# Kernel tuning notes

Hardware: AMD Instinct MI355X
Metric: run time of the kernel (lower is better)

The kernel has to match this reference:

```python
import jax, jax.numpy as jnp
import numpy as np

INPUT_SZ = 16
HPF = 32  # hidden_per_feat_sz
INTERACTIONS = [(0, 1), (2, 3), (4, 5), (6, 7)]
N_INT = len(INTERACTIONS)
INPUT_SIZE = INPUT_SZ + 2 * N_INT          # 24
HIDDEN = (INPUT_SZ + N_INT) * HPF          # 640
BATCH, SEQ = 128, 512

# static masks, faithful to the torch code (note: only even-indexed interactions
# get U_mask rows, exactly as the original loop `range(0, len(interactions), 2)`)
_Um = np.zeros((INPUT_SIZE, HIDDEN), np.float32)
for i in range(INPUT_SZ):
    _Um[i, i * HPF:(i + 1) * HPF] = 1
for i in range(0, N_INT, 2):
    _Um[i + INPUT_SZ, i * HPF:(i + 1) * HPF] = 1
    _Um[i + INPUT_SZ + 1, i * HPF:(i + 1) * HPF] = 1
U_MASK = jnp.asarray(_Um)
V_MASK = jnp.asarray(np.kron(np.eye(INPUT_SZ + N_INT, dtype=np.float32),
                             np.ones((HPF, HPF), np.float32)))
FEAT_SEQ = np.array(list(range(INPUT_SZ)) + [f for p in INTERACTIONS for f in p])


def setup_inputs() -> dict:
    key = jax.random.key(0)
    ks = jax.random.split(key, 13)
    stdv = 1.0 / np.sqrt(HIDDEN)
    u = lambda k, s: jax.random.uniform(k, s, jnp.float32, -stdv, stdv)
    inp = {"x": jax.random.normal(ks[0], (BATCH, SEQ, INPUT_SZ), jnp.float32)}
    names = ["i", "f", "c", "o"]
    for j, n in enumerate(names):
        inp[f"U_{n}"] = u(ks[1 + 3 * j], (INPUT_SIZE, HIDDEN))
        inp[f"V_{n}"] = u(ks[2 + 3 * j], (HIDDEN, HIDDEN))
        inp[f"b_{n}"] = u(ks[3 + 3 * j], (HIDDEN,))
    return inp


def reference(x, U_i, V_i, b_i, U_f, V_f, b_f, U_c, V_c, b_c, U_o, V_o, b_o):
    # gather masked-feature view of inputs once: [B, T, INPUT_SIZE]
    xg = x[:, :, FEAT_SEQ]
    # precompute masked, gate-concatenated weights (i|f|c|o)
    Ucat = jnp.concatenate([U_i * U_MASK, U_f * U_MASK,
                            U_c * U_MASK, U_o * U_MASK], axis=1)   # [in, 4H]
    Vcat = jnp.concatenate([V_i * V_MASK, V_f * V_MASK,
                            V_c * V_MASK, V_o * V_MASK], axis=1)   # [H, 4H]
    bcat = jnp.concatenate([b_i, b_f, b_c, b_o])                   # [4H]
    # input contribution for all timesteps in one GEMM: [B, T, 4H]
    xU = jnp.einsum('bti,ig->btg', xg, Ucat) + bcat

    h0 = jnp.zeros((x.shape[0], HIDDEN), x.dtype)
    c0 = jnp.zeros_like(h0)

    def step(carry, xu_t):
        h, c = carry
        gates = xu_t + h @ Vcat
        i_t, f_t, g_t, o_t = jnp.split(gates, 4, axis=-1)
        c = jax.nn.sigmoid(f_t) * c + jax.nn.sigmoid(i_t) * jnp.tanh(g_t)
        h = jax.nn.sigmoid(o_t) * jnp.tanh(c)
        return (h, c), h

    (h_t, c_t), hs = jax.lax.scan(step, (h0, c0), jnp.swapaxes(xU, 0, 1))
    hidden_seq = jnp.swapaxes(hs, 0, 1)  # [B, T, H]
    return hidden_seq, (h_t, c_t)
```

## Files before the change

kernel.cpp:

```cpp
#include <hip/hip_runtime.h>


#define TT 512
#define HN 640
#define BN 128

typedef float f2 __attribute__((ext_vector_type(2)));

__device__ __forceinline__ float rl(float v, int s) {
  return __int_as_float(__builtin_amdgcn_readlane(__float_as_int(v), s));
}

__global__ __attribute__((amdgpu_flat_work_group_size(64, 64),
                          amdgpu_waves_per_eu(2, 4)))
void lstm_kernel(
    const float* __restrict__ x,
    const float* __restrict__ Ui, const float* __restrict__ Vi, const float* __restrict__ bi,
    const float* __restrict__ Uf, const float* __restrict__ Vf, const float* __restrict__ bf,
    const float* __restrict__ Uc, const float* __restrict__ Vc, const float* __restrict__ bc,
    const float* __restrict__ Uo, const float* __restrict__ Vo, const float* __restrict__ bo,
    float* __restrict__ out) {
  __shared__ __align__(16) float hsh[64];

  const int unit = blockIdx.x;
  const int lane = threadIdx.x;
  const int j = unit >> 7;
  const int b = unit & 127;
  const int gp = lane >> 5;
  const int n = lane & 31;
  const int col = j * 32 + n;

  const float* UG1 = gp ? Uc : Ui;
  const float* UG2 = gp ? Uo : Uf;
  const float* VG1 = gp ? Vc : Vi;
  const float* VG2 = gp ? Vo : Vf;
  const float* bG1 = gp ? bc : bi;
  const float* bG2 = gp ? bo : bf;

  const float LOG2E = 1.44269504088896340736f;
  const float B1 = gp ? (-2.f * LOG2E) : -LOG2E;
  const float B2 = -LOG2E;
  const float Ac1 = gp ? 2.f : 1.f;
  const float Cc1 = gp ? -1.f : 0.f;

  float w11 = 0.f, w21 = 0.f, w12 = 0.f, w22 = 0.f;
  int f1 = 0, f2i = 0;
  if (j < 16) {
    f1 = f2i = j;
    w11 = UG1[j * HN + col];
    w12 = UG2[j * HN + col];
    if (j == 0) {
      w11 += UG1[16 * HN + col]; w12 += UG2[16 * HN + col];
      w21  = UG1[17 * HN + col]; w22  = UG2[17 * HN + col];
      f2i = 1;
    } else if (j == 2) {
      w11 += UG1[18 * HN + col]; w12 += UG2[18 * HN + col];
      w21  = UG1[19 * HN + col]; w22  = UG2[19 * HN + col];
      f2i = 3;
    }
  }
  const float ws11 = B1 * w11, ws21 = B1 * w21, bs1 = B1 * bG1[col];
  const float ws12 = B2 * w12, ws22 = B2 * w22, bs2 = B2 * bG2[col];

  f2 wA[16], wB[16];
#pragma unroll
  for (int kp = 0; kp < 16; ++kp) {
    wA[kp].x = B1 * VG1[(j * 32 + 2 * kp) * HN + col];
    wA[kp].y = B1 * VG1[(j * 32 + 2 * kp + 1) * HN + col];
    wB[kp].x = B2 * VG2[(j * 32 + 2 * kp) * HN + col];
    wB[kp].y = B2 * VG2[(j * 32 + 2 * kp + 1) * HN + col];
  }
#pragma unroll
  for (int kp = 0; kp < 16; ++kp) {
    asm volatile("" : "+v"(wA[kp]), "+v"(wB[kp]));
  }

  float h = 0.f, c = 0.f;
  int ob = b * TT * HN + col;
#pragma unroll 1
  for (int i = 0; i < 8; ++i) {
    const int t = i * 64 + lane;
    float xc1 = x[(b * TT + t) * 16 + f1];
    float xc2 = x[(b * TT + t) * 16 + f2i];
    asm volatile("" : "+v"(xc1), "+v"(xc2));
    for (int s = 0; s < 64; ++s) {
      const float x1 = rl(xc1, s);
      const float x2 = rl(xc2, s);
      const float sx1 = fmaf(x2, ws21, fmaf(x1, ws11, bs1));
      const float sx2 = fmaf(x2, ws22, fmaf(x1, ws12, bs2));
      hsh[lane] = h;
      __builtin_amdgcn_wave_barrier();
      f2 hp[16];
      __builtin_memcpy(hp, hsh, 128);
      __builtin_amdgcn_wave_barrier();
      f2 aA = {sx1, 0.f}, aB = {sx2, 0.f};
#pragma unroll
      for (int kp = 0; kp < 16; ++kp) {
        aA = __builtin_elementwise_fma(wA[kp], hp[kp], aA);
        aB = __builtin_elementwise_fma(wB[kp], hp[kp], aB);
      }
      const float a1 = aA.x + aA.y;
      const float a2 = aB.x + aB.y;
      const float e1 = __builtin_amdgcn_exp2f(a1);
      const float e2 = __builtin_amdgcn_exp2f(a2);
      const float g1 = fmaf(Ac1, __builtin_amdgcn_rcpf(1.f + e1), Cc1);
      const float g2 = __builtin_amdgcn_rcpf(1.f + e2);
      const float p1 = __shfl_xor(g1, 32);
      const float p2 = __shfl_xor(g2, 32);
      c = fmaf(g2, c, g1 * p1);
      const float tc = fmaf(
          2.f,
          __builtin_amdgcn_rcpf(1.f + __builtin_amdgcn_exp2f(-2.f * LOG2E * c)),
          -1.f);
      h = p2 * tc;
      if (lane < 32) out[ob] = h;
      ob += HN;
    }
  }
  if (lane < 32) {
    out[BN * TT * HN + b * HN + col] = h;
    out[BN * TT * HN + BN * HN + b * HN + col] = c;
  }
}

extern "C" void kernel_launch(void* const* d_in, const int* in_sizes, int n_in,
                              void* d_out, int out_size, void* d_ws, size_t ws_size,
                              hipStream_t stream) {
  (void)in_sizes; (void)n_in; (void)d_ws; (void)ws_size; (void)out_size;
  const float* x  = (const float*)d_in[0];
  const float* Ui = (const float*)d_in[1];
  const float* Vi = (const float*)d_in[2];
  const float* bi = (const float*)d_in[3];
  const float* Uf = (const float*)d_in[4];
  const float* Vf = (const float*)d_in[5];
  const float* bf = (const float*)d_in[6];
  const float* Uc = (const float*)d_in[7];
  const float* Vc = (const float*)d_in[8];
  const float* bc = (const float*)d_in[9];
  const float* Uo = (const float*)d_in[10];
  const float* Vo = (const float*)d_in[11];
  const float* bo = (const float*)d_in[12];
  float* out = (float*)d_out;

  dim3 grid(2560);
  dim3 block(64);
  hipLaunchKernelGGL(lstm_kernel, grid, block, 0, stream,
                     x, Ui, Vi, bi, Uf, Vf, bf, Uc, Vc, bc, Uo, Vo, bo, out);
}
```

Measured before the change: 385.0 us.

## Hand-write LSTM timestep loop in inline assembly with LDS-staged inputs

The per-timestep recurrence is replaced by a hand-scheduled inline-asm loop. Inputs are staged in LDS and fetched with ds_read2, replacing readlane. The next 64-step x chunk is prefetched into registers, and the half-wave exchange uses ds_bpermute. Outputs go through buffer_store with an out-of-range offset that masks the upper half-wave, removing the branch. The intent is to shorten the serial per-step latency chain, at the cost of fragile hardcoded registers, s_nop hazard handling and dropping the waves_per_eu hint.

```diff
diff --git a/kernel.cpp b/kernel.cpp
--- a/kernel.cpp
+++ b/kernel.cpp
@@ -6,13 +6,9 @@
 #define BN 128
 
 typedef float f2 __attribute__((ext_vector_type(2)));
-
-__device__ __forceinline__ float rl(float v, int s) {
-  return __int_as_float(__builtin_amdgcn_readlane(__float_as_int(v), s));
-}
-
-__global__ __attribute__((amdgpu_flat_work_group_size(64, 64),
-                          amdgpu_waves_per_eu(2, 4)))
+typedef unsigned int u32x4 __attribute__((ext_vector_type(4)));
+
+__global__ __attribute__((amdgpu_flat_work_group_size(64, 64)))
 void lstm_kernel(
     const float* __restrict__ x,
     const float* __restrict__ Ui, const float* __restrict__ Vi, const float* __restrict__ bi,
@@ -20,7 +16,7 @@
     const float* __restrict__ Uc, const float* __restrict__ Vc, const float* __restrict__ bc,
     const float* __restrict__ Uo, const float* __restrict__ Vo, const float* __restrict__ bo,
     float* __restrict__ out) {
-  __shared__ __align__(16) float hsh[64];
+  __shared__ __align__(16) float hsh[192];
 
   const int unit = blockIdx.x;
   const int lane = threadIdx.x;
@@ -70,53 +66,151 @@
     wB[kp].x = B2 * VG2[(j * 32 + 2 * kp) * HN + col];
     wB[kp].y = B2 * VG2[(j * 32 + 2 * kp + 1) * HN + col];
   }
-#pragma unroll
-  for (int kp = 0; kp < 16; ++kp) {
-    asm volatile("" : "+v"(wA[kp]), "+v"(wB[kp]));
-  }
+
+  const unsigned zb    = (unsigned)(unsigned long long)&hsh[0];
+  const unsigned laddr = zb + (unsigned)lane * 4u;
+  const unsigned xbase = zb + 256u;
+  const unsigned swz   = (unsigned)((lane ^ 32) & 63) * 4u;
+
+  const unsigned out_bytes = (unsigned)((BN * TT * HN + 2 * BN * HN) * 4);
+  const unsigned long long outa = (unsigned long long)out;
+  u32x4 srd;
+  srd.x = (unsigned)outa;
+  srd.y = (unsigned)(outa >> 32);
+  srd.z = out_bytes;
+  srd.w = 0x00020000u;
+  unsigned voff = (lane < 32) ? (unsigned)((b * TT * HN + col) * 4)
+                              : 0x60000000u;
 
   float h = 0.f, c = 0.f;
-  int ob = b * TT * HN + col;
+
+  float nx1 = x[(b * TT + lane) * 16 + f1];
+  float nx2 = x[(b * TT + lane) * 16 + f2i];
+
 #pragma unroll 1
   for (int i = 0; i < 8; ++i) {
-    const int t = i * 64 + lane;
-    float xc1 = x[(b * TT + t) * 16 + f1];
-    float xc2 = x[(b * TT + t) * 16 + f2i];
-    asm volatile("" : "+v"(xc1), "+v"(xc2));
-    for (int s = 0; s < 64; ++s) {
-      const float x1 = rl(xc1, s);
-      const float x2 = rl(xc2, s);
-      const float sx1 = fmaf(x2, ws21, fmaf(x1, ws11, bs1));
-      const float sx2 = fmaf(x2, ws22, fmaf(x1, ws12, bs2));
-      hsh[lane] = h;
-      __builtin_amdgcn_wave_barrier();
-      f2 hp[16];
-      __builtin_memcpy(hp, hsh, 128);
-      __builtin_amdgcn_wave_barrier();
-      f2 aA = {sx1, 0.f}, aB = {sx2, 0.f};
-#pragma unroll
-      for (int kp = 0; kp < 16; ++kp) {
-        aA = __builtin_elementwise_fma(wA[kp], hp[kp], aA);
-        aB = __builtin_elementwise_fma(wB[kp], hp[kp], aB);
-      }
-      const float a1 = aA.x + aA.y;
-      const float a2 = aB.x + aB.y;
-      const float e1 = __builtin_amdgcn_exp2f(a1);
-      const float e2 = __builtin_amdgcn_exp2f(a2);
-      const float g1 = fmaf(Ac1, __builtin_amdgcn_rcpf(1.f + e1), Cc1);
-      const float g2 = __builtin_amdgcn_rcpf(1.f + e2);
-      const float p1 = __shfl_xor(g1, 32);
-      const float p2 = __shfl_xor(g2, 32);
-      c = fmaf(g2, c, g1 * p1);
-      const float tc = fmaf(
-          2.f,
-          __builtin_amdgcn_rcpf(1.f + __builtin_amdgcn_exp2f(-2.f * LOG2E * c)),
-          -1.f);
-      h = p2 * tc;
-      if (lane < 32) out[ob] = h;
-      ob += HN;
+    hsh[64 + lane]  = nx1;
+    hsh[128 + lane] = nx2;
+    if (i < 7) {
+      const int t = (i + 1) * 64 + lane;
+      nx1 = x[(b * TT + t) * 16 + f1];
+      nx2 = x[(b * TT + t) * 16 + f2i];
     }
-  }
+    unsigned xaddr = xbase;
+    asm volatile(
+      "s_mov_b32 s20, 64\n\t"
+      "Lstep%=:\n\t"
+      "ds_write_b32 %[laddr], %[h]\n\t"
+      "ds_read2_b32 v[38:39], %[xaddr] offset0:0 offset1:64\n\t"
+      "ds_read_b128 v[48:51], %[zb]\n\t"
+      "ds_read_b128 v[52:55], %[zb] offset:16\n\t"
+      "ds_read_b128 v[56:59], %[zb] offset:32\n\t"
+      "ds_read_b128 v[60:63], %[zb] offset:48\n\t"
+      "ds_read_b128 v[64:67], %[zb] offset:64\n\t"
+      "ds_read_b128 v[68:71], %[zb] offset:80\n\t"
+      "ds_read_b128 v[72:75], %[zb] offset:96\n\t"
+      "ds_read_b128 v[76:79], %[zb] offset:112\n\t"
+      "v_add_u32 %[xaddr], 4, %[xaddr]\n\t"
+      "s_waitcnt lgkmcnt(8)\n\t"
+      "v_mov_b32 v36, %[bs1]\n\t"
+      "v_fmac_f32 v36, v38, %[w11]\n\t"
+      "v_fmac_f32 v36, v39, %[w21]\n\t"
+      "v_mov_b32 v37, %[bs2]\n\t"
+      "v_fmac_f32 v37, v38, %[w12]\n\t"
+      "v_fmac_f32 v37, v39, %[w22]\n\t"
+      "v_mov_b32 v40, v36\n\t"
+      "v_mov_b32 v41, 0\n\t"
+      "v_mov_b32 v42, 0\n\t"
+      "v_mov_b32 v43, 0\n\t"
+      "v_mov_b32 v44, v37\n\t"
+      "v_mov_b32 v45, 0\n\t"
+      "v_mov_b32 v46, 0\n\t"
+      "v_mov_b32 v47, 0\n\t"
+      "s_waitcnt lgkmcnt(0)\n\t"
+      "v_pk_fma_f32 v[40:41], %[wa0],  v[48:49], v[40:41]\n\t"
+      "v_pk_fma_f32 v[44:45], %[wb0],  v[48:49], v[44:45]\n\t"
+      "v_pk_fma_f32 v[42:43], %[wa1],  v[50:51], v[42:43]\n\t"
+      "v_pk_fma_f32 v[46:47], %[wb1],  v[50:51], v[46:47]\n\t"
+      "v_pk_fma_f32 v[40:41], %[wa2],  v[52:53], v[40:41]\n\t"
+      "v_pk_fma_f32 v[44:45], %[wb2],  v[52:53], v[44:45]\n\t"
+      "v_pk_fma_f32 v[42:43], %[wa3],  v[54:55], v[42:43]\n\t"
+      "v_pk_fma_f32 v[46:47], %[wb3],  v[54:55], v[46:47]\n\t"
+      "v_pk_fma_f32 v[40:41], %[wa4],  v[56:57], v[40:41]\n\t"
+      "v_pk_fma_f32 v[44:45], %[wb4],  v[56:57], v[44:45]\n\t"
+      "v_pk_fma_f32 v[42:43], %[wa5],  v[58:59], v[42:43]\n\t"
+      "v_pk_fma_f32 v[46:47], %[wb5],  v[58:59], v[46:47]\n\t"
+      "v_pk_fma_f32 v[40:41], %[wa6],  v[60:61], v[40:41]\n\t"
+      "v_pk_fma_f32 v[44:45], %[wb6],  v[60:61], v[44:45]\n\t"
+      "v_pk_fma_f32 v[42:43], %[wa7],  v[62:63], v[42:43]\n\t"
+      "v_pk_fma_f32 v[46:47], %[wb7],  v[62:63], v[46:47]\n\t"
+      "v_pk_fma_f32 v[40:41], %[wa8],  v[64:65], v[40:41]\n\t"
+      "v_pk_fma_f32 v[44:45], %[wb8],  v[64:65], v[44:45]\n\t"
+      "v_pk_fma_f32 v[42:43], %[wa9],  v[66:67], v[42:43]\n\t"
+      "v_pk_fma_f32 v[46:47], %[wb9],  v[66:67], v[46:47]\n\t"
+      "v_pk_fma_f32 v[40:41], %[wa10], v[68:69], v[40:41]\n\t"
+      "v_pk_fma_f32 v[44:45], %[wb10], v[68:69], v[44:45]\n\t"
+      "v_pk_fma_f32 v[42:43], %[wa11], v[70:71], v[42:43]\n\t"
+      "v_pk_fma_f32 v[46:47], %[wb11], v[70:71], v[46:47]\n\t"
+      "v_pk_fma_f32 v[40:41], %[wa12], v[72:73], v[40:41]\n\t"
+      "v_pk_fma_f32 v[44:45], %[wb12], v[72:73], v[44:45]\n\t"
+      "v_pk_fma_f32 v[42:43], %[wa13], v[74:75], v[42:43]\n\t"
+      "v_pk_fma_f32 v[46:47], %[wb13], v[74:75], v[46:47]\n\t"
+      "v_pk_fma_f32 v[40:41], %[wa14], v[76:77], v[40:41]\n\t"
+      "v_pk_fma_f32 v[44:45], %[wb14], v[76:77], v[44:45]\n\t"
+      "v_pk_fma_f32 v[42:43], %[wa15], v[78:79], v[42:43]\n\t"
+      "v_pk_fma_f32 v[46:47], %[wb15], v[78:79], v[46:47]\n\t"
+      "v_pk_add_f32 v[40:41], v[40:41], v[42:43]\n\t"
+      "v_pk_add_f32 v[44:45], v[44:45], v[46:47]\n\t"
+      "v_add_f32 v81, v40, v41\n\t"
+      "v_add_f32 v82, v44, v45\n\t"
+      "v_exp_f32 v81, v81\n\t"
+      "v_exp_f32 v82, v82\n\t"
+      "s_nop 1\n\t"
+      "v_add_f32 v81, 1.0, v81\n\t"
+      "v_add_f32 v82, 1.0, v82\n\t"
+      "v_rcp_f32 v81, v81\n\t"
+      "v_rcp_f32 v82, v82\n\t"
+      "s_nop 1\n\t"
+      "v_fma_f32 v81, %[ac1], v81, %[cc1]\n\t"
+      "ds_bpermute_b32 v83, %[swz], v81\n\t"
+      "ds_bpermute_b32 v84, %[swz], v82\n\t"
+      "s_waitcnt lgkmcnt(0)\n\t"
+      "v_mul_f32 v85, v81, v83\n\t"
+      "v_fma_f32 %[c], v82, %[c], v85\n\t"
+      "v_mul_f32 v86, 0xc038aa3b, %[c]\n\t"
+      "v_exp_f32 v86, v86\n\t"
+      "s_nop 1\n\t"
+      "v_add_f32 v86, 1.0, v86\n\t"
+      "v_rcp_f32 v86, v86\n\t"
+      "s_nop 1\n\t"
+      "v_fma_f32 v86, 2.0, v86, -1.0\n\t"
+      "v_mul_f32 %[h], v84, v86\n\t"
+      "buffer_store_dword %[h], %[voff], %[srd], 0 offen\n\t"
+      "v_add_u32 %[voff], 0xa00, %[voff]\n\t"
+      "s_sub_u32 s20, s20, 1\n\t"
+      "s_cmp_lg_u32 s20, 0\n\t"
+      "s_cbranch_scc1 Lstep%=\n\t"
+      : [h]"+v"(h), [c]"+v"(c), [voff]"+v"(voff), [xaddr]"+v"(xaddr)
+      : [laddr]"v"(laddr), [zb]"v"(zb), [swz]"v"(swz),
+        [w11]"v"(ws11), [w21]"v"(ws21), [bs1]"v"(bs1),
+        [w12]"v"(ws12), [w22]"v"(ws22), [bs2]"v"(bs2),
+        [ac1]"v"(Ac1), [cc1]"v"(Cc1), [srd]"s"(srd),
+        [wa0]"v"(wA[0]),  [wa1]"v"(wA[1]),  [wa2]"v"(wA[2]),  [wa3]"v"(wA[3]),
+        [wa4]"v"(wA[4]),  [wa5]"v"(wA[5]),  [wa6]"v"(wA[6]),  [wa7]"v"(wA[7]),
+        [wa8]"v"(wA[8]),  [wa9]"v"(wA[9]),  [wa10]"v"(wA[10]),[wa11]"v"(wA[11]),
+        [wa12]"v"(wA[12]),[wa13]"v"(wA[13]),[wa14]"v"(wA[14]),[wa15]"v"(wA[15]),
+        [wb0]"v"(wB[0]),  [wb1]"v"(wB[1]),  [wb2]"v"(wB[2]),  [wb3]"v"(wB[3]),
+        [wb4]"v"(wB[4]),  [wb5]"v"(wB[5]),  [wb6]"v"(wB[6]),  [wb7]"v"(wB[7]),
+        [wb8]"v"(wB[8]),  [wb9]"v"(wB[9]),  [wb10]"v"(wB[10]),[wb11]"v"(wB[11]),
+        [wb12]"v"(wB[12]),[wb13]"v"(wB[13]),[wb14]"v"(wB[14]),[wb15]"v"(wB[15])
+      : "memory", "scc", "s20",
+        "v36","v37","v38","v39","v40","v41","v42","v43","v44","v45","v46",
+        "v47","v48","v49","v50","v51","v52","v53","v54","v55","v56","v57",
+        "v58","v59","v60","v61","v62","v63","v64","v65","v66","v67","v68",
+        "v69","v70","v71","v72","v73","v74","v75","v76","v77","v78","v79",
+        "v81","v82","v83","v84","v85","v86");
+  }
+
   if (lane < 32) {
     out[BN * TT * HN + b * HN + col] = h;
     out[BN * TT * HN + BN * HN + b * HN + col] = c;
```

Result: no change. 392.2 us (+1.9%).

## Process two batches per wave with all four gates per lane in inline asm

Applied to the files above, without the earlier changes.

Each wave now handles two batch rows (one per half-wave), and every lane computes all four gates for its column instead of splitting gates across half-waves. This removes the cross-half shuffle and halves the grid. The 32x4 block-diagonal weights are staged through LDS into 128 registers. The whole time loop is hand-written inline assembly using packed FMAs, buffer loads/stores and x staged in LDS. The cost is doubled per-lane FMA work and a large register footprint with hard-coded registers, which can limit occupancy and is fragile.

```diff
diff --git a/kernel.cpp b/kernel.cpp
--- a/kernel.cpp
+++ b/kernel.cpp
@@ -6,13 +6,9 @@
 #define BN 128
 
 typedef float f2 __attribute__((ext_vector_type(2)));
-
-__device__ __forceinline__ float rl(float v, int s) {
-  return __int_as_float(__builtin_amdgcn_readlane(__float_as_int(v), s));
-}
-
-__global__ __attribute__((amdgpu_flat_work_group_size(64, 64),
-                          amdgpu_waves_per_eu(2, 4)))
+typedef unsigned int u32x4 __attribute__((ext_vector_type(4)));
+
+__global__ __attribute__((amdgpu_flat_work_group_size(64, 64)))
 void lstm_kernel(
     const float* __restrict__ x,
     const float* __restrict__ Ui, const float* __restrict__ Vi, const float* __restrict__ bi,
@@ -20,107 +16,275 @@
     const float* __restrict__ Uc, const float* __restrict__ Vc, const float* __restrict__ bc,
     const float* __restrict__ Uo, const float* __restrict__ Vo, const float* __restrict__ bo,
     float* __restrict__ out) {
-  __shared__ __align__(16) float hsh[64];
+  __shared__ __align__(16) float lds[4544];
 
   const int unit = blockIdx.x;
   const int lane = threadIdx.x;
-  const int j = unit >> 7;
-  const int b = unit & 127;
+  const int j  = unit >> 6;
+  const int bp = unit & 63;
   const int gp = lane >> 5;
-  const int n = lane & 31;
+  const int n  = lane & 31;
   const int col = j * 32 + n;
-
-  const float* UG1 = gp ? Uc : Ui;
-  const float* UG2 = gp ? Uo : Uf;
-  const float* VG1 = gp ? Vc : Vi;
-  const float* VG2 = gp ? Vo : Vf;
-  const float* bG1 = gp ? bc : bi;
-  const float* bG2 = gp ? bo : bf;
+  const int b  = bp * 2 + gp;
 
   const float LOG2E = 1.44269504088896340736f;
-  const float B1 = gp ? (-2.f * LOG2E) : -LOG2E;
-  const float B2 = -LOG2E;
-  const float Ac1 = gp ? 2.f : 1.f;
-  const float Cc1 = gp ? -1.f : 0.f;
-
-  float w11 = 0.f, w21 = 0.f, w12 = 0.f, w22 = 0.f;
-  int f1 = 0, f2i = 0;
-  if (j < 16) {
-    f1 = f2i = j;
-    w11 = UG1[j * HN + col];
-    w12 = UG2[j * HN + col];
-    if (j == 0) {
-      w11 += UG1[16 * HN + col]; w12 += UG2[16 * HN + col];
-      w21  = UG1[17 * HN + col]; w22  = UG2[17 * HN + col];
-      f2i = 1;
-    } else if (j == 2) {
-      w11 += UG1[18 * HN + col]; w12 += UG2[18 * HN + col];
-      w21  = UG1[19 * HN + col]; w22  = UG2[19 * HN + col];
-      f2i = 3;
+  const float Bs = -LOG2E;
+  const float Bg = -2.f * LOG2E;
+
+  if (lane < 32) {
+    for (int k = 0; k < 32; ++k) {
+      const int r = (j * 32 + k) * HN + col;
+      lds[n * 132 + k * 4 + 0] = Bs * Vi[r];
+      lds[n * 132 + k * 4 + 1] = Bs * Vf[r];
+      lds[n * 132 + k * 4 + 2] = Bg * Vc[r];
+      lds[n * 132 + k * 4 + 3] = Bs * Vo[r];
     }
   }
-  const float ws11 = B1 * w11, ws21 = B1 * w21, bs1 = B1 * bG1[col];
-  const float ws12 = B2 * w12, ws22 = B2 * w22, bs2 = B2 * bG2[col];
-
-  f2 wA[16], wB[16];
-#pragma unroll
-  for (int kp = 0; kp < 16; ++kp) {
-    wA[kp].x = B1 * VG1[(j * 32 + 2 * kp) * HN + col];
-    wA[kp].y = B1 * VG1[(j * 32 + 2 * kp + 1) * HN + col];
-    wB[kp].x = B2 * VG2[(j * 32 + 2 * kp) * HN + col];
-    wB[kp].y = B2 * VG2[(j * 32 + 2 * kp + 1) * HN + col];
-  }
-#pragma unroll
-  for (int kp = 0; kp < 16; ++kp) {
-    asm volatile("" : "+v"(wA[kp]), "+v"(wB[kp]));
-  }
+
+  int f1 = 0, f2i = 0;
+  if (j < 16) { f1 = f2i = j; if (j == 0) f2i = 1; else if (j == 2) f2i = 3; }
+  auto uw = [&](const float* __restrict__ U, float& w1, float& w2) {
+    w1 = 0.f; w2 = 0.f;
+    if (j < 16) {
+      w1 = U[j * HN + col];
+      if (j == 0)      { w1 += U[16 * HN + col]; w2 = U[17 * HN + col]; }
+      else if (j == 2) { w1 += U[18 * HN + col]; w2 = U[19 * HN + col]; }
+    }
+  };
+  float wi1, wi2, wf1, wf2, wg1, wg2, wo1, wo2;
+  uw(Ui, wi1, wi2); uw(Uf, wf1, wf2); uw(Uc, wg1, wg2); uw(Uo, wo1, wo2);
+  const f2 w11IF = {Bs * wi1, Bs * wf1}, w21IF = {Bs * wi2, Bs * wf2};
+  const f2 w11GO = {Bg * wg1, Bs * wo1}, w21GO = {Bg * wg2, Bs * wo2};
+  const f2 bsIF  = {Bs * bi[col], Bs * bf[col]};
+  const f2 bsGO  = {Bg * bc[col], Bs * bo[col]};
+
+  const unsigned zb    = (unsigned)(unsigned long long)&lds[0];
+  const unsigned wrd   = zb + (unsigned)n * 528u;
+  const unsigned laddr = zb + 16896u + (unsigned)lane * 4u;
+  const unsigned hrd   = zb + 16896u + (unsigned)gp * 128u;
+  const unsigned xw    = zb + 17152u + (unsigned)lane * 4u;
+  const unsigned xrb   = zb + 17152u + (unsigned)gp * 512u;
+
+  u32x4 xsrd, osrd;
+  { const unsigned long long a = (unsigned long long)x;
+    xsrd.x = (unsigned)a; xsrd.y = (unsigned)(a >> 32);
+    xsrd.z = (unsigned)(BN * TT * 16 * 4); xsrd.w = 0x00020000u; }
+  { const unsigned long long a = (unsigned long long)out;
+    osrd.x = (unsigned)a; osrd.y = (unsigned)(a >> 32);
+    osrd.z = (unsigned)((BN * TT * HN + 2 * BN * HN) * 4); osrd.w = 0x00020000u; }
+
+  unsigned voff  = (unsigned)((b * TT * HN + col) * 4);
+  unsigned xvoff = (unsigned)((((bp * 2) * TT + lane) * 16 + f1) * 4);
+  const int sfd  = (f2i - f1) * 4;
 
   float h = 0.f, c = 0.f;
-  int ob = b * TT * HN + col;
-#pragma unroll 1
-  for (int i = 0; i < 8; ++i) {
-    const int t = i * 64 + lane;
-    float xc1 = x[(b * TT + t) * 16 + f1];
-    float xc2 = x[(b * TT + t) * 16 + f2i];
-    asm volatile("" : "+v"(xc1), "+v"(xc2));
-    for (int s = 0; s < 64; ++s) {
-      const float x1 = rl(xc1, s);
-      const float x2 = rl(xc2, s);
-      const float sx1 = fmaf(x2, ws21, fmaf(x1, ws11, bs1));
-      const float sx2 = fmaf(x2, ws22, fmaf(x1, ws12, bs2));
-      hsh[lane] = h;
-      __builtin_amdgcn_wave_barrier();
-      f2 hp[16];
-      __builtin_memcpy(hp, hsh, 128);
-      __builtin_amdgcn_wave_barrier();
-      f2 aA = {sx1, 0.f}, aB = {sx2, 0.f};
-#pragma unroll
-      for (int kp = 0; kp < 16; ++kp) {
-        aA = __builtin_elementwise_fma(wA[kp], hp[kp], aA);
-        aB = __builtin_elementwise_fma(wB[kp], hp[kp], aB);
-      }
-      const float a1 = aA.x + aA.y;
-      const float a2 = aB.x + aB.y;
-      const float e1 = __builtin_amdgcn_exp2f(a1);
-      const float e2 = __builtin_amdgcn_exp2f(a2);
-      const float g1 = fmaf(Ac1, __builtin_amdgcn_rcpf(1.f + e1), Cc1);
-      const float g2 = __builtin_amdgcn_rcpf(1.f + e2);
-      const float p1 = __shfl_xor(g1, 32);
-      const float p2 = __shfl_xor(g2, 32);
-      c = fmaf(g2, c, g1 * p1);
-      const float tc = fmaf(
-          2.f,
-          __builtin_amdgcn_rcpf(1.f + __builtin_amdgcn_exp2f(-2.f * LOG2E * c)),
-          -1.f);
-      h = p2 * tc;
-      if (lane < 32) out[ob] = h;
-      ob += HN;
-    }
-  }
-  if (lane < 32) {
-    out[BN * TT * HN + b * HN + col] = h;
-    out[BN * TT * HN + BN * HN + b * HN + col] = c;
-  }
+
+  asm volatile(
+    "s_waitcnt lgkmcnt(0)\n\t"
+    "ds_read_b128 v[96:99],   %[wrd]\n\t"
+    "ds_read_b128 v[100:103], %[wrd] offset:16\n\t"
+    "ds_read_b128 v[104:107], %[wrd] offset:32\n\t"
+    "ds_read_b128 v[108:111], %[wrd] offset:48\n\t"
+    "ds_read_b128 v[112:115], %[wrd] offset:64\n\t"
+    "ds_read_b128 v[116:119], %[wrd] offset:80\n\t"
+    "ds_read_b128 v[120:123], %[wrd] offset:96\n\t"
+    "ds_read_b128 v[124:127], %[wrd] offset:112\n\t"
+    "ds_read_b128 v[128:131], %[wrd] offset:128\n\t"
+    "ds_read_b128 v[132:135], %[wrd] offset:144\n\t"
+    "ds_read_b128 v[136:139], %[wrd] offset:160\n\t"
+    "ds_read_b128 v[140:143], %[wrd] offset:176\n\t"
+    "ds_read_b128 v[144:147], %[wrd] offset:192\n\t"
+    "ds_read_b128 v[148:151], %[wrd] offset:208\n\t"
+    "ds_read_b128 v[152:155], %[wrd] offset:224\n\t"
+    "ds_read_b128 v[156:159], %[wrd] offset:240\n\t"
+    "ds_read_b128 v[160:163], %[wrd] offset:256\n\t"
+    "ds_read_b128 v[164:167], %[wrd] offset:272\n\t"
+    "ds_read_b128 v[168:171], %[wrd] offset:288\n\t"
+    "ds_read_b128 v[172:175], %[wrd] offset:304\n\t"
+    "ds_read_b128 v[176:179], %[wrd] offset:320\n\t"
+    "ds_read_b128 v[180:183], %[wrd] offset:336\n\t"
+    "ds_read_b128 v[184:187], %[wrd] offset:352\n\t"
+    "ds_read_b128 v[188:191], %[wrd] offset:368\n\t"
+    "ds_read_b128 v[192:195], %[wrd] offset:384\n\t"
+    "ds_read_b128 v[196:199], %[wrd] offset:400\n\t"
+    "ds_read_b128 v[200:203], %[wrd] offset:416\n\t"
+    "ds_read_b128 v[204:207], %[wrd] offset:432\n\t"
+    "ds_read_b128 v[208:211], %[wrd] offset:448\n\t"
+    "ds_read_b128 v[212:215], %[wrd] offset:464\n\t"
+    "ds_read_b128 v[216:219], %[wrd] offset:480\n\t"
+    "ds_read_b128 v[220:223], %[wrd] offset:496\n\t"
+    "s_mov_b32 s22, 0x8000\n\t"
+    "s_add_u32 s23, s22, %[sfd]\n\t"
+    "buffer_load_dword v36, %[xvoff], %[xsrd], 0 offen\n\t"
+    "buffer_load_dword v37, %[xvoff], %[xsrd], %[sfd] offen\n\t"
+    "buffer_load_dword v38, %[xvoff], %[xsrd], s22 offen\n\t"
+    "buffer_load_dword v39, %[xvoff], %[xsrd], s23 offen\n\t"
+    "s_mov_b32 s21, 8\n\t"
+    "Lchunk%=:\n\t"
+    "s_waitcnt vmcnt(0)\n\t"
+    "ds_write_b32 %[xw], v36\n\t"
+    "ds_write_b32 %[xw], v37 offset:256\n\t"
+    "ds_write_b32 %[xw], v38 offset:512\n\t"
+    "ds_write_b32 %[xw], v39 offset:768\n\t"
+    "v_add_u32 %[xvoff], 0x1000, %[xvoff]\n\t"
+    "buffer_load_dword v36, %[xvoff], %[xsrd], 0 offen\n\t"
+    "buffer_load_dword v37, %[xvoff], %[xsrd], %[sfd] offen\n\t"
+    "buffer_load_dword v38, %[xvoff], %[xsrd], s22 offen\n\t"
+    "buffer_load_dword v39, %[xvoff], %[xsrd], s23 offen\n\t"
+    "v_mov_b32 v33, %[xrb]\n\t"
+    "s_mov_b32 s20, 64\n\t"
+    "Lstep%=:\n\t"
+    "ds_write_b32 %[laddr], %[h]\n\t"
+    "ds_read2_b32 v[88:89], v33 offset0:0 offset1:64\n\t"
+    "ds_read_b128 v[48:51], %[hrd]\n\t"
+    "ds_read_b128 v[52:55], %[hrd] offset:16\n\t"
+    "ds_read_b128 v[56:59], %[hrd] offset:32\n\t"
+    "ds_read_b128 v[60:63], %[hrd] offset:48\n\t"
+    "ds_read_b128 v[64:67], %[hrd] offset:64\n\t"
+    "ds_read_b128 v[68:71], %[hrd] offset:80\n\t"
+    "ds_read_b128 v[72:75], %[hrd] offset:96\n\t"
+    "ds_read_b128 v[76:79], %[hrd] offset:112\n\t"
+    "v_add_u32 v33, 4, v33\n\t"
+    "s_waitcnt lgkmcnt(8)\n\t"
+    "v_pk_fma_f32 v[40:41], v[88:89], %[w11IF], %[bsIF] op_sel:[0,0,0] op_sel_hi:[0,1,1]\n\t"
+    "v_pk_fma_f32 v[44:45], v[88:89], %[w11GO], %[bsGO] op_sel:[0,0,0] op_sel_hi:[0,1,1]\n\t"
+    "v_pk_fma_f32 v[40:41], v[88:89], %[w21IF], v[40:41] op_sel:[1,0,0] op_sel_hi:[1,1,1]\n\t"
+    "v_pk_fma_f32 v[44:45], v[88:89], %[w21GO], v[44:45] op_sel:[1,0,0] op_sel_hi:[1,1,1]\n\t"
+    "v_mov_b32 v42, 0\n\t"
+    "v_mov_b32 v43, 0\n\t"
+    "v_mov_b32 v46, 0\n\t"
+    "v_mov_b32 v47, 0\n\t"
+    "s_waitcnt lgkmcnt(0)\n\t"
+    "v_pk_fma_f32 v[40:41], v[96:97],   v[48:49], v[40:41] op_sel:[0,0,0] op_sel_hi:[1,0,1]\n\t"
+    "v_pk_fma_f32 v[44:45], v[98:99],   v[48:49], v[44:45] op_sel:[0,0,0] op_sel_hi:[1,0,1]\n\t"
+    "v_pk_fma_f32 v[42:43], v[100:101], v[48:49], v[42:43] op_sel:[0,1,0] op_sel_hi:[1,1,1]\n\t"
+    "v_pk_fma_f32 v[46:47], v[102:103], v[48:49], v[46:47] op_sel:[0,1,0] op_sel_hi:[1,1,1]\n\t"
+    "v_pk_fma_f32 v[40:41], v[104:105], v[50:51], v[40:41] op_sel:[0,0,0] op_sel_hi:[1,0,1]\n\t"
+    "v_pk_fma_f32 v[44:45], v[106:107], v[50:51], v[44:45] op_sel:[0,0,0] op_sel_hi:[1,0,1]\n\t"
+    "v_pk_fma_f32 v[42:43], v[108:109], v[50:51], v[42:43] op_sel:[0,1,0] op_sel_hi:[1,1,1]\n\t"
+    "v_pk_fma_f32 v[46:47], v[110:111], v[50:51], v[46:47] op_sel:[0,1,0] op_sel_hi:[1,1,1]\n\t"
+    "v_pk_fma_f32 v[40:41], v[112:113], v[52:53], v[40:41] op_sel:[0,0,0] op_sel_hi:[1,0,1]\n\t"
+    "v_pk_fma_f32 v[44:45], v[114:115], v[52:53], v[44:45] op_sel:[0,0,0] op_sel_hi:[1,0,1]\n\t"
+    "v_pk_fma_f32 v[42:43], v[116:117], v[52:53], v[42:43] op_sel:[0,1,0] op_sel_hi:[1,1,1]\n\t"
+    "v_pk_fma_f32 v[46:47], v[118:119], v[52:53], v[46:47] op_sel:[0,1,0] op_sel_hi:[1,1,1]\n\t"
+    "v_pk_fma_f32 v[40:41], v[120:121], v[54:55], v[40:41] op_sel:[0,0,0] op_sel_hi:[1,0,1]\n\t"
+    "v_pk_fma_f32 v[44:45], v[122:123], v[54:55], v[44:45] op_sel:[0,0,0] op_sel_hi:[1,0,1]\n\t"
+    "v_pk_fma_f32 v[42:43], v[124:125], v[54:55], v[42:43] op_sel:[0,1,0] op_sel_hi:[1,1,1]\n\t"
+    "v_pk_fma_f32 v[46:47], v[126:127], v[54:55], v[46:47] op_sel:[0,1,0] op_sel_hi:[1,1,1]\n\t"
+    "v_pk_fma_f32 v[40:41], v[128:129], v[56:57], v[40:41] op_sel:[0,0,0] op_sel_hi:[1,0,1]\n\t"
+    "v_pk_fma_f32 v[44:45], v[130:131], v[56:57], v[44:45] op_sel:[0,0,0] op_sel_hi:[1,0,1]\n\t"
+    "v_pk_fma_f32 v[42:43], v[132:133], v[56:57], v[42:43] op_sel:[0,1,0] op_sel_hi:[1,1,1]\n\t"
+    "v_pk_fma_f32 v[46:47], v[134:135], v[56:57], v[46:47] op_sel:[0,1,0] op_sel_hi:[1,1,1]\n\t"
+    "v_pk_fma_f32 v[40:41], v[136:137], v[58:59], v[40:41] op_sel:[0,0,0] op_sel_hi:[1,0,1]\n\t"
+    "v_pk_fma_f32 v[44:45], v[138:139], v[58:59], v[44:45] op_sel:[0,0,0] op_sel_hi:[1,0,1]\n\t"
+    "v_pk_fma_f32 v[42:43], v[140:141], v[58:59], v[42:43] op_sel:[0,1,0] op_sel_hi:[1,1,1]\n\t"
+    "v_pk_fma_f32 v[46:47], v[142:143], v[58:59], v[46:47] op_sel:[0,1,0] op_sel_hi:[1,1,1]\n\t"
+    "v_pk_fma_f32 v[40:41], v[144:145], v[60:61], v[40:41] op_sel:[0,0,0] op_sel_hi:[1,0,1]\n\t"
+    "v_pk_fma_f32 v[44:45], v[146:147], v[60:61], v[44:45] op_sel:[0,0,0] op_sel_hi:[1,0,1]\n\t"
+    "v_pk_fma_f32 v[42:43], v[148:149], v[60:61], v[42:43] op_sel:[0,1,0] op_sel_hi:[1,1,1]\n\t"
+    "v_pk_fma_f32 v[46:47], v[150:151], v[60:61], v[46:47] op_sel:[0,1,0] op_sel_hi:[1,1,1]\n\t"
+    "v_pk_fma_f32 v[40:41], v[152:153], v[62:63], v[40:41] op_sel:[0,0,0] op_sel_hi:[1,0,1]\n\t"
+    "v_pk_fma_f32 v[44:45], v[154:155], v[62:63], v[44:45] op_sel:[0,0,0] op_sel_hi:[1,0,1]\n\t"
+    "v_pk_fma_f32 v[42:43], v[156:157], v[62:63], v[42:43] op_sel:[0,1,0] op_sel_hi:[1,1,1]\n\t"
+    "v_pk_fma_f32 v[46:47], v[158:159], v[62:63], v[46:47] op_sel:[0,1,0] op_sel_hi:[1,1,1]\n\t"
+    "v_pk_fma_f32 v[40:41], v[160:161], v[64:65], v[40:41] op_sel:[0,0,0] op_sel_hi:[1,0,1]\n\t"
+    "v_pk_fma_f32 v[44:45], v[162:163], v[64:65], v[44:45] op_sel:[0,0,0] op_sel_hi:[1,0,1]\n\t"
+    "v_pk_fma_f32 v[42:43], v[164:165], v[64:65], v[42:43] op_sel:[0,1,0] op_sel_hi:[1,1,1]\n\t"
+    "v_pk_fma_f32 v[46:47], v[166:167], v[64:65], v[46:47] op_sel:[0,1,0] op_sel_hi:[1,1,1]\n\t"
+    "v_pk_fma_f32 v[40:41], v[168:169], v[66:67], v[40:41] op_sel:[0,0,0] op_sel_hi:[1,0,1]\n\t"
+    "v_pk_fma_f32 v[44:45], v[170:171], v[66:67], v[44:45] op_sel:[0,0,0] op_sel_hi:[1,0,1]\n\t"
+    "v_pk_fma_f32 v[42:43], v[172:173], v[66:67], v[42:43] op_sel:[0,1,0] op_sel_hi:[1,1,1]\n\t"
+    "v_pk_fma_f32 v[46:47], v[174:175], v[66:67], v[46:47] op_sel:[0,1,0] op_sel_hi:[1,1,1]\n\t"
+    "v_pk_fma_f32 v[40:41], v[176:177], v[68:69], v[40:41] op_sel:[0,0,0] op_sel_hi:[1,0,1]\n\t"
+    "v_pk_fma_f32 v[44:45], v[178:179], v[68:69], v[44:45] op_sel:[0,0,0] op_sel_hi:[1,0,1]\n\t"
+    "v_pk_fma_f32 v[42:43], v[180:181], v[68:69], v[42:43] op_sel:[0,1,0] op_sel_hi:[1,1,1]\n\t"
+    "v_pk_fma_f32 v[46:47], v[182:183], v[68:69], v[46:47] op_sel:[0,1,0] op_sel_hi:[1,1,1]\n\t"
+    "v_pk_fma_f32 v[40:41], v[184:185], v[70:71], v[40:41] op_sel:[0,0,0] op_sel_hi:[1,0,1]\n\t"
+    "v_pk_fma_f32 v[44:45], v[186:187], v[70:71], v[44:45] op_sel:[0,0,0] op_sel_hi:[1,0,1]\n\t"
+    "v_pk_fma_f32 v[42:43], v[188:189], v[70:71], v[42:43] op_sel:[0,1,0] op_sel_hi:[1,1,1]\n\t"
+    "v_pk_fma_f32 v[46:47], v[190:191], v[70:71], v[46:47] op_sel:[0,1,0] op_sel_hi:[1,1,1]\n\t"
+    "v_pk_fma_f32 v[40:41], v[192:193], v[72:73], v[40:41] op_sel:[0,0,0] op_sel_hi:[1,0,1]\n\t"
+    "v_pk_fma_f32 v[44:45], v[194:195], v[72:73], v[44:45] op_sel:[0,0,0] op_sel_hi:[1,0,1]\n\t"
+    "v_pk_fma_f32 v[42:43], v[196:197], v[72:73], v[42:43] op_sel:[0,1,0] op_sel_hi:[1,1,1]\n\t"
+    "v_pk_fma_f32 v[46:47], v[198:199], v[72:73], v[46:47] op_sel:[0,1,0] op_sel_hi:[1,1,1]\n\t"
+    "v_pk_fma_f32 v[40:41], v[200:201], v[74:75], v[40:41] op_sel:[0,0,0] op_sel_hi:[1,0,1]\n\t"
+    "v_pk_fma_f32 v[44:45], v[202:203], v[74:75], v[44:45] op_sel:[0,0,0] op_sel_hi:[1,0,1]\n\t"
+    "v_pk_fma_f32 v[42:43], v[204:205], v[74:75], v[42:43] op_sel:[0,1,0] op_sel_hi:[1,1,1]\n\t"
+    "v_pk_fma_f32 v[46:47], v[206:207], v[74:75], v[46:47] op_sel:[0,1,0] op_sel_hi:[1,1,1]\n\t"
+    "v_pk_fma_f32 v[40:41], v[208:209], v[76:77], v[40:41] op_sel:[0,0,0] op_sel_hi:[1,0,1]\n\t"
+    "v_pk_fma_f32 v[44:45], v[210:211], v[76:77], v[44:45] op_sel:[0,0,0] op_sel_hi:[1,0,1]\n\t"
+    "v_pk_fma_f32 v[42:43], v[212:213], v[76:77], v[42:43] op_sel:[0,1,0] op_sel_hi:[1,1,1]\n\t"
+    "v_pk_fma_f32 v[46:47], v[214:215], v[76:77], v[46:47] op_sel:[0,1,0] op_sel_hi:[1,1,1]\n\t"
+    "v_pk_fma_f32 v[40:41], v[216:217], v[78:79], v[40:41] op_sel:[0,0,0] op_sel_hi:[1,0,1]\n\t"
+    "v_pk_fma_f32 v[44:45], v[218:219], v[78:79], v[44:45] op_sel:[0,0,0] op_sel_hi:[1,0,1]\n\t"
+    "v_pk_fma_f32 v[42:43], v[220:221], v[78:79], v[42:43] op_sel:[0,1,0] op_sel_hi:[1,1,1]\n\t"
+    "v_pk_fma_f32 v[46:47], v[222:223], v[78:79], v[46:47] op_sel:[0,1,0] op_sel_hi:[1,1,1]\n\t"
+    "v_pk_add_f32 v[40:41], v[40:41], v[42:43]\n\t"
+    "v_pk_add_f32 v[44:45], v[44:45], v[46:47]\n\t"
+    "v_exp_f32 v80, v40\n\t"
+    "v_exp_f32 v81, v41\n\t"
+    "v_exp_f32 v82, v44\n\t"
+    "v_exp_f32 v83, v45\n\t"
+    "v_add_f32 v80, 1.0, v80\n\t"
+    "v_add_f32 v81, 1.0, v81\n\t"
+    "v_add_f32 v82, 1.0, v82\n\t"
+    "v_add_f32 v83, 1.0, v83\n\t"
+    "v_rcp_f32 v80, v80\n\t"
+    "v_rcp_f32 v81, v81\n\t"
+    "v_rcp_f32 v82, v82\n\t"
+    "v_rcp_f32 v83, v83\n\t"
+    "v_fma_f32 v82, 2.0, v82, -1.0\n\t"
+    "v_mul_f32 v84, v80, v82\n\t"
+    "v_fma_f32 %[c], v81, %[c], v84\n\t"
+    "v_mul_f32 v85, 0xc038aa3b, %[c]\n\t"
+    "v_exp_f32 v85, v85\n\t"
+    "s_nop 1\n\t"
+    "v_add_f32 v85, 1.0, v85\n\t"
+    "v_rcp_f32 v85, v85\n\t"
+    "s_nop 1\n\t"
+    "v_fma_f32 v85, 2.0, v85, -1.0\n\t"
+    "v_mul_f32 %[h], v83, v85\n\t"
+    "buffer_store_dword %[h], %[voff], %[osrd], 0 offen\n\t"
+    "v_add_u32 %[voff], 0xa00, %[voff]\n\t"
+    "s_sub_u32 s20, s20, 1\n\t"
+    "s_cmp_lg_u32 s20, 0\n\t"
+    "s_cbranch_scc1 Lstep%=\n\t"
+    "s_sub_u32 s21, s21, 1\n\t"
+    "s_cmp_lg_u32 s21, 0\n\t"
+    "s_cbranch_scc1 Lchunk%=\n\t"
+    : [h]"+v"(h), [c]"+v"(c), [voff]"+v"(voff), [xvoff]"+v"(xvoff)
+    : [laddr]"v"(laddr), [hrd]"v"(hrd), [xw]"v"(xw), [xrb]"v"(xrb),
+      [wrd]"v"(wrd),
+      [w11IF]"v"(w11IF), [w21IF]"v"(w21IF), [bsIF]"v"(bsIF),
+      [w11GO]"v"(w11GO), [w21GO]"v"(w21GO), [bsGO]"v"(bsGO),
+      [xsrd]"s"(xsrd), [osrd]"s"(osrd), [sfd]"s"(sfd)
+    : "memory", "scc", "s20", "s21", "s22", "s23",
+      "v33","v36","v37","v38","v39",
+      "v40","v41","v42","v43","v44","v45","v46","v47",
+      "v48","v49","v50","v51","v52","v53","v54","v55",
+      "v56","v57","v58","v59","v60","v61","v62","v63",
+      "v64","v65","v66","v67","v68","v69","v70","v71",
+      "v72","v73","v74","v75","v76","v77","v78","v79",
+      "v80","v81","v82","v83","v84","v85","v88","v89",
+      "v96","v97","v98","v99","v100","v101","v102","v103",
+      "v104","v105","v106","v107","v108","v109","v110","v111",
+      "v112","v113","v114","v115","v116","v117","v118","v119",
+      "v120","v121","v122","v123","v124","v125","v126","v127",
+      "v128","v129","v130","v131","v132","v133","v134","v135",
+      "v136","v137","v138","v139","v140","v141","v142","v143",
+      "v144","v145","v146","v147","v148","v149","v150","v151",
+      "v152","v153","v154","v155","v156","v157","v158","v159",
+      "v160","v161","v162","v163","v164","v165","v166","v167",
+      "v168","v169","v170","v171","v172","v173","v174","v175",
+      "v176","v177","v178","v179","v180","v181","v182","v183",
+      "v184","v185","v186","v187","v188","v189","v190","v191",
+      "v192","v193","v194","v195","v196","v197","v198","v199",
+      "v200","v201","v202","v203","v204","v205","v206","v207",
+      "v208","v209","v210","v211","v212","v213","v214","v215",
+      "v216","v217","v218","v219","v220","v221","v222","v223");
+
+  out[BN * TT * HN + b * HN + col] = h;
+  out[BN * TT * HN + BN * HN + b * HN + col] = c;
 }
 
 extern "C" void kernel_launch(void* const* d_in, const int* in_sizes, int n_in,
@@ -142,7 +306,7 @@
   const float* bo = (const float*)d_in[12];
   float* out = (float*)d_out;
 
-  dim3 grid(2560);
+  dim3 grid(1280);
   dim3 block(64);
   hipLaunchKernelGGL(lstm_kernel, grid, block, 0, stream,
                      x, Ui, Vi, bi, Uf, Vf, bf, Uc, Vc, bc, Uo, Vo, bo, out);
```

Result: no change. 390.4 us (+1.4%).
